# Optimization experiments

Hardware: AMD Instinct MI355X
Metric: run time of the kernel (lower is better)

The kernel has to match this reference:

```python
import jax, jax.numpy as jnp
import numpy as np

N_WORDS = 500000
N_LABELS = 64
PAD_INDEX = 0
UNK_INDEX = 1
BATCH, SEQ_LEN = 8192, 512


def setup_inputs() -> dict:
    key = jax.random.key(0)
    kw, kl, klen = jax.random.split(key, 3)
    # sequence lengths in [S/2, S]; pads go at the end (loop semantics assume contiguous prefix)
    lens = jax.random.randint(klen, (BATCH,), SEQ_LEN // 2, SEQ_LEN + 1)
    words = jax.random.randint(kw, (BATCH, SEQ_LEN), 2, N_WORDS, dtype=jnp.int32)
    labels = jax.random.randint(kl, (BATCH, SEQ_LEN), 0, N_LABELS, dtype=jnp.int32)
    pos = jnp.arange(SEQ_LEN, dtype=jnp.int32)[None, :]
    words = jnp.where(pos < lens[:, None], words, PAD_INDEX)
    trans_count = jnp.zeros((N_LABELS + 1, N_LABELS + 1), jnp.float32)
    emit_count = jnp.zeros((N_WORDS, N_LABELS), jnp.float32)
    return {"words": words, "labels": labels,
            "trans_count": trans_count, "emit_count": emit_count}


def reference(words, labels, trans_count, emit_count):
    # Vectorized equivalent of the double Python loop of scalar increments.
    B, S = words.shape
    lens = (words != PAD_INDEX).sum(-1)                       # [B]
    valid = jnp.arange(S, dtype=lens.dtype)[None, :] < lens[:, None]  # [B,S]
    wgt = valid.astype(trans_count.dtype).ravel()             # 1.0 for counted tokens
    ext_words = jnp.where(words >= N_WORDS, UNK_INDEX, words)
    # pre label: -1 (== last index N_LABELS) at j=0, else labels[:, j-1]
    pre = jnp.concatenate(
        [jnp.full((B, 1), N_LABELS, labels.dtype), labels[:, :-1]], axis=1)
    # trans_count[t, pre] += 1  (flattened scatter-add)
    t_flat = (labels.astype(jnp.int32) * (N_LABELS + 1) + pre.astype(jnp.int32)).ravel()
    tc = trans_count.ravel().at[t_flat].add(wgt).reshape(trans_count.shape)
    # emit_count[w, t] += 1
    e_flat = (ext_words.astype(jnp.int32) * N_LABELS + labels.astype(jnp.int32)).ravel()
    ec = emit_count.ravel().at[e_flat].add(wgt).reshape(emit_count.shape)
    return tc, ec
```

## Files before the change

kernel.cpp:

```cpp
#include <hip/hip_runtime.h>
#include <hip/hip_bf16.h>


constexpr int N_WORDS  = 500000;
constexpr int N_LABELS = 64;
constexpr int SEQ_LEN  = 512;
constexpr int BINS     = (N_LABELS + 1) * (N_LABELS + 1);
constexpr int N_CELLS  = N_WORDS * N_LABELS;
constexpr int P        = 1000;
constexpr int CPP      = 32000;
constexpr int TILE_TOK = 4096;
constexpr int QPT      = TILE_TOK / 4;
constexpr int B1 = 1024, G1 = 512;
constexpr int B2 = 1024;
constexpr int FIN_BLOCKS = 5;


__global__ __launch_bounds__(B1)
void phase1(const int* __restrict__ words, const int* __restrict__ labels,
            unsigned* __restrict__ dir,
            unsigned short* __restrict__ keys,
            unsigned* __restrict__ part_t,
            int n, int ntiles) {
    __shared__ unsigned trans[BINS];
    __shared__ unsigned keybuf[TILE_TOK];
    __shared__ unsigned short sorted[TILE_TOK];
    __shared__ unsigned cnt[1024];
    __shared__ unsigned wsum[16];
    const int tid  = threadIdx.x;
    const int lane = tid & 63;
    for (int k = tid; k < BINS; k += B1) trans[k] = 0u;

    const int nquads = n >> 2;
    for (int tile = blockIdx.x; tile < ntiles; tile += gridDim.x) {
        const int q0 = tile * QPT;
        const int tq = min(QPT, nquads - q0);
        cnt[tid] = 0u;
        __syncthreads();

        if (tid < tq) {
            const int q = q0 + tid;
            const int i = q << 2;
            const int4 w4 = reinterpret_cast<const int4*>(words)[q];
            const int4 l4 = reinterpret_cast<const int4*>(labels)[q];
            const int j0 = i & (SEQ_LEN - 1);
            int pre = (j0 == 0) ? N_LABELS : labels[i - 1];
            int wv[4] = {w4.x, w4.y, w4.z, w4.w};
            int lv[4] = {l4.x, l4.y, l4.z, l4.w};
            unsigned pk[4];
            #pragma unroll
            for (int k = 0; k < 4; ++k) {
                const int lab = lv[k];
                unsigned pack = 0xFFFFFFFFu;
                if (wv[k] != 0) {
                    atomicAdd(&trans[lab * (N_LABELS + 1) + pre], 1u);
                    const int w = (wv[k] >= N_WORDS) ? 1 : wv[k];
                    const unsigned key = (unsigned)w * N_LABELS + (unsigned)lab;
                    const unsigned p   = key / CPP;
                    pack = (p << 16) | (key - p * CPP);
                    atomicAdd(&cnt[p], 1u);
                }
                pk[k] = pack;
                pre = lab;
            }
            reinterpret_cast<uint4*>(keybuf)[tid] = make_uint4(pk[0], pk[1], pk[2], pk[3]);
        }
        __syncthreads();

        {
            const unsigned c = cnt[tid];
            unsigned v = c;
            #pragma unroll
            for (int d = 1; d < 64; d <<= 1) {
                const unsigned u = __shfl_up(v, d, 64);
                if (lane >= d) v += u;
            }
            if (lane == 63) wsum[tid >> 6] = v;
            __syncthreads();
            if (tid < 16) {
                const unsigned s = wsum[tid];
                unsigned vv = s;
                #pragma unroll
                for (int d = 1; d < 16; d <<= 1) {
                    const unsigned u = __shfl_up(vv, d, 64);
                    if (tid >= d) vv += u;
                }
                wsum[tid] = vv - s;
            }
            __syncthreads();
            const unsigned off = v - c + wsum[tid >> 6];
            cnt[tid] = off;
            if (tid < P) dir[(size_t)tile * P + tid] = (c << 16) | off;
        }
        __syncthreads();

        const int tt = tq << 2;
        for (int t = tid; t < tt; t += B1) {
            const unsigned pack = keybuf[t];
            if (pack != 0xFFFFFFFFu) {
                const unsigned s = atomicAdd(&cnt[pack >> 16], 1u);
                sorted[s] = (unsigned short)(pack & 0xFFFFu);
            }
        }
        __syncthreads();

        if (tid < TILE_TOK / 8)
            reinterpret_cast<uint4*>(keys + (size_t)tile * TILE_TOK)[tid] =
                reinterpret_cast<const uint4*>(sorted)[tid];
        __syncthreads();
    }

    unsigned* my = part_t + (size_t)blockIdx.x * BINS;
    for (int k = tid; k < BINS; k += B1) my[k] = trans[k];
}


__global__ __launch_bounds__(256)
void transpose_dir(const unsigned* __restrict__ dir, unsigned* __restrict__ dirT,
                   int ntiles, int tstride) {
    __shared__ unsigned tb[32][33];
    const int p0 = blockIdx.x * 32, t0 = blockIdx.y * 32;
    const int tx = threadIdx.x, ty = threadIdx.y;
    for (int j = ty; j < 32; j += 8) {
        const int t = t0 + j, p = p0 + tx;
        tb[j][tx] = (t < ntiles && p < P) ? dir[(size_t)t * P + p] : 0u;
    }
    __syncthreads();
    for (int j = ty; j < 32; j += 8) {
        const int p = p0 + j, t = t0 + tx;
        if (p < P && t < tstride) dirT[(size_t)p * tstride + t] = tb[tx][j];
    }
}


__global__ __launch_bounds__(B2)
void phase2(const unsigned* __restrict__ dirT,
            const unsigned short* __restrict__ keys,
            const unsigned* __restrict__ part_t,
            float* __restrict__ out, int ntiles, int tstride) {
    extern __shared__ unsigned h[];
    const unsigned bid = blockIdx.x;

    if (bid < (unsigned)FIN_BLOCKS) {
        const int k = bid * B2 + threadIdx.x;
        if (k < BINS) {
            unsigned s = 0;
            #pragma unroll 8
            for (int pb = 0; pb < G1; ++pb) s += part_t[(size_t)pb * BINS + k];
            out[k] = (float)s;
        }
        return;
    }
    const unsigned p = bid - FIN_BLOCKS;

    for (int j = threadIdx.x; j < CPP / 2; j += B2) h[j] = 0u;
    __syncthreads();

    const unsigned* drow = dirT + (size_t)p * tstride;
    for (int t = threadIdx.x; t < ntiles; t += B2) {
        const unsigned e = drow[t];
        unsigned c = e >> 16;
        const unsigned short* kp = keys + (size_t)t * TILE_TOK + (e & 0xFFFFu);
        for (unsigned i = 0; i < c; ++i) {
            const unsigned loc = kp[i];
            atomicAdd(&h[loc >> 1], (loc & 1u) ? 65536u : 1u);
        }
    }
    __syncthreads();

    float* __restrict__ emit = out + BINS;
    float* dst = emit + (size_t)p * CPP;
    if (threadIdx.x < 3)
        dst[threadIdx.x] =
            (float)((h[threadIdx.x >> 1] >> ((threadIdx.x & 1u) * 16)) & 0xFFFFu);
    if (threadIdx.x == 3)
        dst[CPP - 1] = (float)(h[(CPP - 1) >> 1] >> 16);
    float4* dst4 = reinterpret_cast<float4*>(dst + 3);
    for (int u = threadIdx.x; u < (CPP - 4) / 4; u += B2) {
        const unsigned w0 = h[2 * u + 1];
        const unsigned w1 = h[2 * u + 2];
        const unsigned w2 = h[2 * u + 3];
        float4 f;
        f.x = (float)(w0 >> 16);
        f.y = (float)(w1 & 0xFFFFu);
        f.z = (float)(w1 >> 16);
        f.w = (float)(w2 & 0xFFFFu);
        dst4[u] = f;
    }
}


__global__ __launch_bounds__(256)
void zero_kernel(uint4* __restrict__ out, int out_quads, int out_size) {
    const uint4 z = {0u, 0u, 0u, 0u};
    const int stride = gridDim.x * blockDim.x;
    for (int q = blockIdx.x * blockDim.x + threadIdx.x; q < out_quads; q += stride)
        out[q] = z;
    if (blockIdx.x == 0 && threadIdx.x < (out_size & 3))
        ((unsigned*)out)[(out_quads << 2) + threadIdx.x] = 0u;
}

__global__ __launch_bounds__(1024)
void count_fallback(const int* __restrict__ words, const int* __restrict__ labels,
                    float* __restrict__ out, int nquads) {
    __shared__ unsigned hist[BINS];
    for (int k = threadIdx.x; k < BINS; k += 1024) hist[k] = 0u;
    __syncthreads();
    float* __restrict__ emit = out + BINS;
    const int stride = gridDim.x * blockDim.x;
    for (int q = blockIdx.x * blockDim.x + threadIdx.x; q < nquads; q += stride) {
        const int i = q << 2;
        const int4 w4 = reinterpret_cast<const int4*>(words)[q];
        const int4 l4 = reinterpret_cast<const int4*>(labels)[q];
        const int j0 = i & (SEQ_LEN - 1);
        int pre = (j0 == 0) ? N_LABELS : labels[i - 1];
        int wv[4] = {w4.x, w4.y, w4.z, w4.w};
        int lv[4] = {l4.x, l4.y, l4.z, l4.w};
        #pragma unroll
        for (int k = 0; k < 4; ++k) {
            const int w = wv[k], lab = lv[k];
            if (w != 0) {
                atomicAdd(&hist[lab * (N_LABELS + 1) + pre], 1u);
                const int we = (w >= N_WORDS) ? 1 : w;
                atomicAdd(&emit[(size_t)we * N_LABELS + lab], 1.0f);
            }
            pre = lab;
        }
    }
    __syncthreads();
    for (int k = threadIdx.x; k < BINS; k += 1024) {
        const unsigned c = hist[k];
        if (c) atomicAdd(&out[k], (float)c);
    }
}


extern "C" void kernel_launch(void* const* d_in, const int* in_sizes, int n_in,
                              void* d_out, int out_size, void* d_ws, size_t ws_size,
                              hipStream_t stream) {
    const int* words  = (const int*)d_in[0];
    const int* labels = (const int*)d_in[1];
    float* out = (float*)d_out;
    const int n = in_sizes[0];

    const int nquads  = n >> 2;
    const int ntiles  = (nquads + QPT - 1) / QPT;
    const int tstride = ((ntiles + 63) / 64) * 64;

    const size_t dir_bytes  = (size_t)ntiles * P * sizeof(unsigned);
    const size_t dirT_bytes = (size_t)P * tstride * sizeof(unsigned);
    const size_t key_bytes  = (size_t)ntiles * TILE_TOK * sizeof(unsigned short);
    const size_t part_bytes = (size_t)G1 * BINS * sizeof(unsigned);
    const size_t dir_off  = 0;
    const size_t dirT_off = dir_off + ((dir_bytes + 255) & ~size_t(255));
    const size_t key_off  = dirT_off + ((dirT_bytes + 255) & ~size_t(255));
    const size_t part_off = key_off + ((key_bytes + 255) & ~size_t(255));
    const size_t need     = part_off + part_bytes;

    if (ws_size >= need) {
        unsigned*       dir    = (unsigned*)((char*)d_ws + dir_off);
        unsigned*       dirT   = (unsigned*)((char*)d_ws + dirT_off);
        unsigned short* keys   = (unsigned short*)((char*)d_ws + key_off);
        unsigned*       part_t = (unsigned*)((char*)d_ws + part_off);

        phase1<<<G1, B1, 0, stream>>>(words, labels, dir, keys, part_t, n, ntiles);
        dim3 tg((P + 31) / 32, (tstride + 31) / 32);
        transpose_dir<<<tg, dim3(32, 8), 0, stream>>>(dir, dirT, ntiles, tstride);
        phase2<<<P + FIN_BLOCKS, B2, (CPP / 2) * sizeof(unsigned), stream>>>(
            dirT, keys, part_t, out, ntiles, tstride);
    } else {
        const int out_quads = out_size >> 2;
        zero_kernel<<<2048, 256, 0, stream>>>((uint4*)d_out, out_quads, out_size);
        count_fallback<<<512, 1024, 0, stream>>>(words, labels, out, nquads);
    }
}
```

Baseline: 254.5 us.

## Drop directory transpose kernel, use 512-thread phase1 blocks with one tile per block

```diff
diff --git a/kernel.cpp b/kernel.cpp
--- a/kernel.cpp
+++ b/kernel.cpp
@@ -11,7 +11,8 @@
 constexpr int CPP      = 32000;
 constexpr int TILE_TOK = 4096;
 constexpr int QPT      = TILE_TOK / 4;
-constexpr int B1 = 1024, G1 = 512;
+constexpr int B1 = 512;
+constexpr int MAXT = 1024;
 constexpr int B2 = 1024;
 constexpr int FIN_BLOCKS = 5;
 
@@ -26,20 +27,21 @@
     __shared__ unsigned keybuf[TILE_TOK];
     __shared__ unsigned short sorted[TILE_TOK];
     __shared__ unsigned cnt[1024];
-    __shared__ unsigned wsum[16];
+    __shared__ unsigned wsum[8];
     const int tid  = threadIdx.x;
     const int lane = tid & 63;
+    const int wid  = tid >> 6;
     for (int k = tid; k < BINS; k += B1) trans[k] = 0u;
 
     const int nquads = n >> 2;
     for (int tile = blockIdx.x; tile < ntiles; tile += gridDim.x) {
         const int q0 = tile * QPT;
         const int tq = min(QPT, nquads - q0);
-        cnt[tid] = 0u;
-        __syncthreads();
-
-        if (tid < tq) {
-            const int q = q0 + tid;
+        cnt[tid] = 0u; cnt[tid + 512] = 0u;
+        __syncthreads();
+
+        for (int lq = tid; lq < tq; lq += B1) {
+            const int q = q0 + lq;
             const int i = q << 2;
             const int4 w4 = reinterpret_cast<const int4*>(words)[q];
             const int4 l4 = reinterpret_cast<const int4*>(labels)[q];
@@ -63,34 +65,38 @@
                 pk[k] = pack;
                 pre = lab;
             }
-            reinterpret_cast<uint4*>(keybuf)[tid] = make_uint4(pk[0], pk[1], pk[2], pk[3]);
+            reinterpret_cast<uint4*>(keybuf)[lq] = make_uint4(pk[0], pk[1], pk[2], pk[3]);
         }
         __syncthreads();
 
         {
-            const unsigned c = cnt[tid];
-            unsigned v = c;
+            const unsigned c0 = cnt[2 * tid], c1 = cnt[2 * tid + 1];
+            const unsigned s  = c0 + c1;
+            unsigned v = s;
             #pragma unroll
             for (int d = 1; d < 64; d <<= 1) {
                 const unsigned u = __shfl_up(v, d, 64);
                 if (lane >= d) v += u;
             }
-            if (lane == 63) wsum[tid >> 6] = v;
+            if (lane == 63) wsum[wid] = v;
             __syncthreads();
-            if (tid < 16) {
-                const unsigned s = wsum[tid];
-                unsigned vv = s;
+            if (tid < 8) {
+                const unsigned sv = wsum[tid];
+                unsigned vv = sv;
                 #pragma unroll
-                for (int d = 1; d < 16; d <<= 1) {
+                for (int d = 1; d < 8; d <<= 1) {
                     const unsigned u = __shfl_up(vv, d, 64);
                     if (tid >= d) vv += u;
                 }
-                wsum[tid] = vv - s;
+                wsum[tid] = vv - sv;
             }
             __syncthreads();
-            const unsigned off = v - c + wsum[tid >> 6];
-            cnt[tid] = off;
-            if (tid < P) dir[(size_t)tile * P + tid] = (c << 16) | off;
+            const unsigned ex = v - s + wsum[wid];
+            cnt[2 * tid]     = ex;
+            cnt[2 * tid + 1] = ex + c0;
+            if (2 * tid + 1 < P)
+                reinterpret_cast<uint2*>(dir + (size_t)tile * P)[tid] =
+                    make_uint2((c0 << 16) | ex, (c1 << 16) | (ex + c0));
         }
         __syncthreads();
 
@@ -104,9 +110,8 @@
         }
         __syncthreads();
 
-        if (tid < TILE_TOK / 8)
-            reinterpret_cast<uint4*>(keys + (size_t)tile * TILE_TOK)[tid] =
-                reinterpret_cast<const uint4*>(sorted)[tid];
+        reinterpret_cast<uint4*>(keys + (size_t)tile * TILE_TOK)[tid] =
+            reinterpret_cast<const uint4*>(sorted)[tid];
         __syncthreads();
     }
 
@@ -115,29 +120,11 @@
 }
 
 
-__global__ __launch_bounds__(256)
-void transpose_dir(const unsigned* __restrict__ dir, unsigned* __restrict__ dirT,
-                   int ntiles, int tstride) {
-    __shared__ unsigned tb[32][33];
-    const int p0 = blockIdx.x * 32, t0 = blockIdx.y * 32;
-    const int tx = threadIdx.x, ty = threadIdx.y;
-    for (int j = ty; j < 32; j += 8) {
-        const int t = t0 + j, p = p0 + tx;
-        tb[j][tx] = (t < ntiles && p < P) ? dir[(size_t)t * P + p] : 0u;
-    }
-    __syncthreads();
-    for (int j = ty; j < 32; j += 8) {
-        const int p = p0 + j, t = t0 + tx;
-        if (p < P && t < tstride) dirT[(size_t)p * tstride + t] = tb[tx][j];
-    }
-}
-
-
 __global__ __launch_bounds__(B2)
-void phase2(const unsigned* __restrict__ dirT,
+void phase2(const unsigned* __restrict__ dir,
             const unsigned short* __restrict__ keys,
             const unsigned* __restrict__ part_t,
-            float* __restrict__ out, int ntiles, int tstride) {
+            float* __restrict__ out, int ntiles, int g1) {
     extern __shared__ unsigned h[];
     const unsigned bid = blockIdx.x;
 
@@ -145,20 +132,19 @@
         const int k = bid * B2 + threadIdx.x;
         if (k < BINS) {
             unsigned s = 0;
-            #pragma unroll 8
-            for (int pb = 0; pb < G1; ++pb) s += part_t[(size_t)pb * BINS + k];
+            for (int pb = 0; pb < g1; ++pb) s += part_t[(size_t)pb * BINS + k];
             out[k] = (float)s;
         }
         return;
     }
     const unsigned p = bid - FIN_BLOCKS;
 
-    for (int j = threadIdx.x; j < CPP / 2; j += B2) h[j] = 0u;
-    __syncthreads();
-
-    const unsigned* drow = dirT + (size_t)p * tstride;
+    for (int j = threadIdx.x; j < CPP / 8; j += B2)
+        reinterpret_cast<uint4*>(h)[j] = make_uint4(0u, 0u, 0u, 0u);
+    __syncthreads();
+
     for (int t = threadIdx.x; t < ntiles; t += B2) {
-        const unsigned e = drow[t];
+        const unsigned e = dir[(size_t)t * P + p];
         unsigned c = e >> 16;
         const unsigned short* kp = keys + (size_t)t * TILE_TOK + (e & 0xFFFFu);
         for (unsigned i = 0; i < c; ++i) {
@@ -243,31 +229,26 @@
     float* out = (float*)d_out;
     const int n = in_sizes[0];
 
-    const int nquads  = n >> 2;
-    const int ntiles  = (nquads + QPT - 1) / QPT;
-    const int tstride = ((ntiles + 63) / 64) * 64;
+    const int nquads = n >> 2;
+    const int ntiles = (nquads + QPT - 1) / QPT;
+    const int g1     = ntiles < MAXT ? ntiles : MAXT;
 
     const size_t dir_bytes  = (size_t)ntiles * P * sizeof(unsigned);
-    const size_t dirT_bytes = (size_t)P * tstride * sizeof(unsigned);
     const size_t key_bytes  = (size_t)ntiles * TILE_TOK * sizeof(unsigned short);
-    const size_t part_bytes = (size_t)G1 * BINS * sizeof(unsigned);
+    const size_t part_bytes = (size_t)g1 * BINS * sizeof(unsigned);
     const size_t dir_off  = 0;
-    const size_t dirT_off = dir_off + ((dir_bytes + 255) & ~size_t(255));
-    const size_t key_off  = dirT_off + ((dirT_bytes + 255) & ~size_t(255));
+    const size_t key_off  = dir_off + ((dir_bytes + 255) & ~size_t(255));
     const size_t part_off = key_off + ((key_bytes + 255) & ~size_t(255));
     const size_t need     = part_off + part_bytes;
 
     if (ws_size >= need) {
         unsigned*       dir    = (unsigned*)((char*)d_ws + dir_off);
-        unsigned*       dirT   = (unsigned*)((char*)d_ws + dirT_off);
         unsigned short* keys   = (unsigned short*)((char*)d_ws + key_off);
         unsigned*       part_t = (unsigned*)((char*)d_ws + part_off);
 
-        phase1<<<G1, B1, 0, stream>>>(words, labels, dir, keys, part_t, n, ntiles);
-        dim3 tg((P + 31) / 32, (tstride + 31) / 32);
-        transpose_dir<<<tg, dim3(32, 8), 0, stream>>>(dir, dirT, ntiles, tstride);
+        phase1<<<g1, B1, 0, stream>>>(words, labels, dir, keys, part_t, n, ntiles);
         phase2<<<P + FIN_BLOCKS, B2, (CPP / 2) * sizeof(unsigned), stream>>>(
-            dirT, keys, part_t, out, ntiles, tstride);
+            dir, keys, part_t, out, ntiles, g1);
     } else {
         const int out_quads = out_size >> 2;
         zero_kernel<<<2048, 256, 0, stream>>>((uint4*)d_out, out_quads, out_size);
```

After: 375.6 us. +47.6%, slower.
